# Optimization experiments

Hardware: AMD Instinct MI355X
Metric: run time of the kernel (lower is better)

Reference implementation:

```python
import jax, jax.numpy as jnp
import numpy as np

N = 100000
E = 1600000
NODE_IN = 8
EDGE_IN = 4
HID = 64
OUT = 4

# torch-initialized skip weights, in usage order (w2_1..w7_7)
SKIP_INIT = np.array([0.6, 0.4,
                      0.6, 0.4, 0.2,
                      0.6, 0.4, 0.2, 0.2,
                      0.6, 0.4, 0.2, 0.2, 0.2,
                      0.6, 0.4, 0.2, 0.2, 0.2, 0.2,
                      0.6, 0.4, 0.2, 0.2, 0.2, 0.2, 0.2], dtype=np.float32)

def _lin(key, fan_in, fan_out):
    b = 1.0 / np.sqrt(fan_in)
    k1, k2 = jax.random.split(key)
    W = jax.random.uniform(k1, (fan_in, fan_out), jnp.float32, -b, b)
    bias = jax.random.uniform(k2, (fan_out,), jnp.float32, -b, b)
    return W, bias

def setup_inputs() -> dict:
    key = jax.random.key(0)
    ks = jax.random.split(key, 20)
    x = jax.random.normal(ks[0], (N, NODE_IN), jnp.float32)
    edge_index = jax.random.randint(ks[1], (2, E), 0, N, jnp.int64)
    edge_attr = jax.random.normal(ks[2], (E, EDGE_IN), jnp.float32)
    # layer1
    Wm1, bm1 = _lin(ks[3], NODE_IN + EDGE_IN, HID)
    Wu1, bu1 = _lin(ks[4], NODE_IN + HID, HID)
    # mid layers (layers 2..6 of the torch module; layer7 is never used)
    Wm_mid, bm_mid, Wu_mid, bu_mid = [], [], [], []
    for i in range(5):
        Wm, bm = _lin(ks[5 + 2 * i], HID + EDGE_IN, HID)
        Wu, bu = _lin(ks[6 + 2 * i], HID + HID, HID)
        Wm_mid.append(Wm); bm_mid.append(bm); Wu_mid.append(Wu); bu_mid.append(bu)
    Wm_mid = jnp.stack(Wm_mid); bm_mid = jnp.stack(bm_mid)
    Wu_mid = jnp.stack(Wu_mid); bu_mid = jnp.stack(bu_mid)
    # last layer
    Wm_last, bm_last = _lin(ks[16], HID + EDGE_IN, OUT)
    Wu_last, bu_last = _lin(ks[17], HID + OUT, OUT)
    skip_weights = jnp.asarray(SKIP_INIT)
    return dict(x=x, edge_index=edge_index, edge_attr=edge_attr,
                Wm1=Wm1, bm1=bm1, Wu1=Wu1, bu1=bu1,
                Wm_mid=Wm_mid, bm_mid=bm_mid, Wu_mid=Wu_mid, bu_mid=bu_mid,
                Wm_last=Wm_last, bm_last=bm_last, Wu_last=Wu_last, bu_last=bu_last,
                skip_weights=skip_weights)

def _graph_layer(h, src, dst, edge_attr, Wm, bm, Wu, bu):
    # message: ReLU(Linear([h_src, e_attr]))  -> [E, out]
    m = jax.nn.relu(jnp.concatenate([h[src], edge_attr], axis=-1) @ Wm + bm)
    # sum-aggregate messages at destination nodes -> [N, out]
    agg = jax.ops.segment_sum(m, dst, num_segments=N)
    # node update: ReLU(Linear([h, agg]))
    return jax.nn.relu(jnp.concatenate([h, agg], axis=-1) @ Wu + bu)

def reference(x, edge_index, edge_attr,
              Wm1, bm1, Wu1, bu1,
              Wm_mid, bm_mid, Wu_mid, bu_mid,
              Wm_last, bm_last, Wu_last, bu_last,
              skip_weights):
    src, dst = edge_index[0], edge_index[1]
    sw = skip_weights
    L = lambda h, i: _graph_layer(h, src, dst, edge_attr,
                                  Wm_mid[i], bm_mid[i], Wu_mid[i], bu_mid[i])
    x1 = _graph_layer(x, src, dst, edge_attr, Wm1, bm1, Wu1, bu1)
    x2 = L(x1, 0)
    x2w = x1 * sw[0] + x2 * sw[1]
    x3 = L(x2w, 1)
    x3w = x1 * sw[2] + x2w * sw[3] + x3 * sw[4]
    x4 = L(x3w, 2)
    x4w = x1 * sw[5] + x2w * sw[6] + x3w * sw[7] + x4 * sw[8]
    x5 = L(x4w, 2)  # NOTE: source reuses layer4 here (faithful to bug)
    x5w = x1 * sw[9] + x2w * sw[10] + x3w * sw[11] + x4w * sw[12] + x5 * sw[13]
    x6 = L(x5w, 3)  # layer5
    x6w = x1 * sw[14] + x2w * sw[15] + x3w * sw[16] + x4w * sw[17] + x5w * sw[18] + x6 * sw[19]
    x7 = L(x6w, 4)  # layer6
    x7w = (x1 * sw[20] + x2w * sw[21] + x3w * sw[22] + x4w * sw[23]
           + x5w * sw[24] + x6w * sw[25] + x7 * sw[26])
    return _graph_layer(x7w, src, dst, edge_attr, Wm_last, bm_last, Wu_last, bu_last)
```

## Files before the change

### kernel.cpp

```cpp
#include <hip/hip_runtime.h>


#define WAVE 64

__global__ __launch_bounds__(256) void hist_kernel(
    const int* __restrict__ ei, int* __restrict__ cnt, int E)
{
    int t = blockIdx.x * blockDim.x + threadIdx.x;
    int nt = gridDim.x * blockDim.x;
    for (int e = t; e < E; e += nt) atomicAdd(&cnt[ei[E + e]], 1);
}

__global__ __launch_bounds__(256) void scan1_kernel(
    const int* __restrict__ cnt, int* __restrict__ out, int* __restrict__ bsum, int N)
{
    __shared__ int lds[256];
    int t = threadIdx.x;
    int base = blockIdx.x * 1024 + t * 4;
    int v0 = (base + 0 < N) ? cnt[base + 0] : 0;
    int v1 = (base + 1 < N) ? cnt[base + 1] : 0;
    int v2 = (base + 2 < N) ? cnt[base + 2] : 0;
    int v3 = (base + 3 < N) ? cnt[base + 3] : 0;
    int tsum = v0 + v1 + v2 + v3;
    lds[t] = tsum;
    __syncthreads();
    for (int off = 1; off < 256; off <<= 1) {
        int x = 0;
        if (t >= off) x = lds[t - off];
        __syncthreads();
        if (t >= off) lds[t] += x;
        __syncthreads();
    }
    int run = lds[t] - tsum;
    if (base + 0 < N) out[base + 0] = run; run += v0;
    if (base + 1 < N) out[base + 1] = run; run += v1;
    if (base + 2 < N) out[base + 2] = run; run += v2;
    if (base + 3 < N) out[base + 3] = run;
    if (t == 255) bsum[blockIdx.x] = lds[255];
}

__global__ __launch_bounds__(256) void scan2_kernel(int* __restrict__ bsum, int B)
{
    __shared__ int lds[256];
    __shared__ int carry;
    int t = threadIdx.x;
    if (t == 0) carry = 0;
    __syncthreads();
    for (int start = 0; start < B; start += 256) {
        int i = start + t;
        int v = (i < B) ? bsum[i] : 0;
        lds[t] = v;
        __syncthreads();
        for (int off = 1; off < 256; off <<= 1) {
            int x = 0;
            if (t >= off) x = lds[t - off];
            __syncthreads();
            if (t >= off) lds[t] += x;
            __syncthreads();
        }
        if (i < B) bsum[i] = carry + lds[t] - v;
        __syncthreads();
        if (t == 255) carry += lds[255];
        __syncthreads();
    }
}

__global__ __launch_bounds__(256) void scan3_kernel(
    int* __restrict__ rowptr, int* __restrict__ cursor,
    const int* __restrict__ bsum, int N, int E)
{
    int t = blockIdx.x * blockDim.x + threadIdx.x;
    int nt = gridDim.x * blockDim.x;
    for (int i = t; i < N; i += nt) {
        int v = rowptr[i] + bsum[i >> 10];
        rowptr[i] = v;
        cursor[i] = v;
    }
    if (t == 0) rowptr[N] = E;
}

__global__ __launch_bounds__(256) void scatter_kernel(
    const int* __restrict__ ei, const float* __restrict__ ea,
    int* __restrict__ cursor, int* __restrict__ srcp, float* __restrict__ eap, int E)
{
    int t = blockIdx.x * blockDim.x + threadIdx.x;
    int nt = gridDim.x * blockDim.x;
    for (int e = t; e < E; e += nt) {
        int d = ei[E + e];
        int pos = atomicAdd(&cursor[d], 1);
        srcp[pos] = ei[e];
        *reinterpret_cast<float4*>(eap + (size_t)4 * pos) =
            *reinterpret_cast<const float4*>(ea + (size_t)4 * e);
    }
}


template<int C>
__device__ __forceinline__ void stage_rows(
    const float* __restrict__ src, int rs, int base, int N, int t, float* As)
{
    constexpr int NFQ = C / 4;
    for (int idx = t; idx < 64 * NFQ; idx += 256) {
        int n = idx / NFQ, kq = idx % NFQ;
        int gn = min(base + n, N - 1);
        *reinterpret_cast<float4*>(As + n * 68 + 4 * kq) =
            *reinterpret_cast<const float4*>(src + (size_t)gn * rs + 4 * kq);
    }
}

template<int C>
__device__ __forceinline__ void stage_w(
    const float* __restrict__ Wg, int t, float* Ws)
{
    const float4* wsrc = reinterpret_cast<const float4*>(Wg);
    float4* wdst = reinterpret_cast<float4*>(Ws);
    for (int idx = t; idx < C * 16; idx += 256) wdst[idx] = wsrc[idx];
}

template<int C>
__device__ __forceinline__ void compute_rm(
    const float* As, const float* Ws, int tx, int ty, float acc[4][4])
{
#pragma unroll 2
    for (int k = 0; k < C; k += 4) {
        float4 w0 = *reinterpret_cast<const float4*>(Ws + (k + 0) * 64 + 4 * tx);
        float4 w1 = *reinterpret_cast<const float4*>(Ws + (k + 1) * 64 + 4 * tx);
        float4 w2 = *reinterpret_cast<const float4*>(Ws + (k + 2) * 64 + 4 * tx);
        float4 w3 = *reinterpret_cast<const float4*>(Ws + (k + 3) * 64 + 4 * tx);
#pragma unroll
        for (int i = 0; i < 4; ++i) {
            float4 a = *reinterpret_cast<const float4*>(As + (4 * ty + i) * 68 + k);
            acc[i][0] = fmaf(a.x, w0.x, acc[i][0]);
            acc[i][1] = fmaf(a.x, w0.y, acc[i][1]);
            acc[i][2] = fmaf(a.x, w0.z, acc[i][2]);
            acc[i][3] = fmaf(a.x, w0.w, acc[i][3]);
            acc[i][0] = fmaf(a.y, w1.x, acc[i][0]);
            acc[i][1] = fmaf(a.y, w1.y, acc[i][1]);
            acc[i][2] = fmaf(a.y, w1.z, acc[i][2]);
            acc[i][3] = fmaf(a.y, w1.w, acc[i][3]);
            acc[i][0] = fmaf(a.z, w2.x, acc[i][0]);
            acc[i][1] = fmaf(a.z, w2.y, acc[i][1]);
            acc[i][2] = fmaf(a.z, w2.z, acc[i][2]);
            acc[i][3] = fmaf(a.z, w2.w, acc[i][3]);
            acc[i][0] = fmaf(a.w, w3.x, acc[i][0]);
            acc[i][1] = fmaf(a.w, w3.y, acc[i][1]);
            acc[i][2] = fmaf(a.w, w3.z, acc[i][2]);
            acc[i][3] = fmaf(a.w, w3.w, acc[i][3]);
        }
    }
}

template<int K1, bool HASB, bool RELU, bool SKIPP, bool UPDP, bool INITP>
__global__ __launch_bounds__(256) void lin3_kernel(
    const float* __restrict__ A, const float* __restrict__ B,
    const float* __restrict__ W, const float* __restrict__ bias,
    float* __restrict__ out, float* __restrict__ P, int N,
    const float* __restrict__ sw, int csIdx, int ciIdx)
{
    __shared__ float As[64 * 68];
    __shared__ float Ws[64 * 64];
    int t = threadIdx.x;
    int tx = t & 15, ty = t >> 4;
    int base = blockIdx.x * 64;

    float acc[4][4];
    {
        float4 bv = *reinterpret_cast<const float4*>(bias + 4 * tx);
#pragma unroll
        for (int i = 0; i < 4; ++i) {
            acc[i][0] = bv.x; acc[i][1] = bv.y; acc[i][2] = bv.z; acc[i][3] = bv.w;
        }
    }

    stage_rows<K1>(A, K1, base, N, t, As);
    stage_w<K1>(W, t, Ws);
    __syncthreads();
    compute_rm<K1>(As, Ws, tx, ty, acc);

    if constexpr (HASB) {
        __syncthreads();
        stage_rows<64>(B, 64, base, N, t, As);
        stage_w<64>(W + (size_t)K1 * 64, t, Ws);
        __syncthreads();
        compute_rm<64>(As, Ws, tx, ty, acc);
    }

    float cs = 0.0f, ci = 0.0f;
    if (SKIPP) cs = sw[csIdx];
    if (UPDP || INITP) ci = sw[ciIdx];

#pragma unroll
    for (int i = 0; i < 4; ++i) {
        int gn = base + 4 * ty + i;
        if (gn >= N) continue;
        float r0 = acc[i][0], r1 = acc[i][1], r2 = acc[i][2], r3 = acc[i][3];
        if (RELU) {
            r0 = fmaxf(r0, 0.0f); r1 = fmaxf(r1, 0.0f);
            r2 = fmaxf(r2, 0.0f); r3 = fmaxf(r3, 0.0f);
        }
        size_t off = (size_t)gn * 64 + 4 * tx;
        float4 Pv;
        if (SKIPP) {
            Pv = *reinterpret_cast<const float4*>(P + off);
            r0 = fmaf(cs, r0, Pv.x);
            r1 = fmaf(cs, r1, Pv.y);
            r2 = fmaf(cs, r2, Pv.z);
            r3 = fmaf(cs, r3, Pv.w);
        }
        float4 r; r.x = r0; r.y = r1; r.z = r2; r.w = r3;
        *reinterpret_cast<float4*>(out + off) = r;
        if (UPDP) {
            float4 Pn;
            Pn.x = fmaf(ci, r0, Pv.x);
            Pn.y = fmaf(ci, r1, Pv.y);
            Pn.z = fmaf(ci, r2, Pv.z);
            Pn.w = fmaf(ci, r3, Pv.w);
            *reinterpret_cast<float4*>(P + off) = Pn;
        }
        if (INITP) {
            float4 Pn;
            Pn.x = ci * r0; Pn.y = ci * r1; Pn.z = ci * r2; Pn.w = ci * r3;
            *reinterpret_cast<float4*>(P + off) = Pn;
        }
    }
}

__global__ __launch_bounds__(256) void csr_agg_kernel(
    const int* __restrict__ rowptr, const int* __restrict__ srcp,
    const float* __restrict__ eap, const float* __restrict__ p,
    const float* __restrict__ Wme, float* __restrict__ agg, int N)
{
    int lane = threadIdx.x & 63;
    int g = lane >> 4;
    int q = lane & 15;
    int gwave = blockIdx.x * (blockDim.x >> 6) + (threadIdx.x >> 6);
    int nw = gridDim.x * (blockDim.x >> 6);
    float4 w0 = *reinterpret_cast<const float4*>(Wme + 0 * 64 + 4 * q);
    float4 w1 = *reinterpret_cast<const float4*>(Wme + 1 * 64 + 4 * q);
    float4 w2 = *reinterpret_cast<const float4*>(Wme + 2 * 64 + 4 * q);
    float4 w3 = *reinterpret_cast<const float4*>(Wme + 3 * 64 + 4 * q);

    for (int n = gwave; n < N; n += nw) {
        int beg = rowptr[n], end = rowptr[n + 1];
        int deg = end - beg;
        int nc = (deg + 3) >> 2;
        float4 acc = {0, 0, 0, 0};
        int sA = 0, sB = 0;
        float4 aA = {0, 0, 0, 0}, aB = {0, 0, 0, 0};
        bool vA = (g < deg);
        bool vB = (4 + g < deg);
        if (vA) { sA = srcp[beg + g];     aA = *reinterpret_cast<const float4*>(eap + (size_t)4 * (beg + g)); }
        if (vB) { sB = srcp[beg + 4 + g]; aB = *reinterpret_cast<const float4*>(eap + (size_t)4 * (beg + 4 + g)); }
        float4 pA = *reinterpret_cast<const float4*>(p + (size_t)sA * 64 + 4 * q);
        for (int c = 0; c < nc; ++c) {
            int sC = 0; float4 aC = {0, 0, 0, 0};
            bool vC = (4 * (c + 2) + g) < deg;
            if (vC) {
                int jc = beg + 4 * (c + 2) + g;
                sC = srcp[jc];
                aC = *reinterpret_cast<const float4*>(eap + (size_t)4 * jc);
            }
            float4 pB = *reinterpret_cast<const float4*>(p + (size_t)sB * 64 + 4 * q);
            float4 m;
            m.x = fmaf(aA.x, w0.x, fmaf(aA.y, w1.x, fmaf(aA.z, w2.x, fmaf(aA.w, w3.x, pA.x))));
            m.y = fmaf(aA.x, w0.y, fmaf(aA.y, w1.y, fmaf(aA.z, w2.y, fmaf(aA.w, w3.y, pA.y))));
            m.z = fmaf(aA.x, w0.z, fmaf(aA.y, w1.z, fmaf(aA.z, w2.z, fmaf(aA.w, w3.z, pA.z))));
            m.w = fmaf(aA.x, w0.w, fmaf(aA.y, w1.w, fmaf(aA.z, w2.w, fmaf(aA.w, w3.w, pA.w))));
            float f = vA ? 1.0f : 0.0f;
            acc.x = fmaf(f, fmaxf(m.x, 0.0f), acc.x);
            acc.y = fmaf(f, fmaxf(m.y, 0.0f), acc.y);
            acc.z = fmaf(f, fmaxf(m.z, 0.0f), acc.z);
            acc.w = fmaf(f, fmaxf(m.w, 0.0f), acc.w);
            vA = vB; aA = aB; pA = pB;
            vB = vC; aB = aC; sB = sC;
        }
        acc.x += __shfl_xor(acc.x, 16); acc.y += __shfl_xor(acc.y, 16);
        acc.z += __shfl_xor(acc.z, 16); acc.w += __shfl_xor(acc.w, 16);
        acc.x += __shfl_xor(acc.x, 32); acc.y += __shfl_xor(acc.y, 32);
        acc.z += __shfl_xor(acc.z, 32); acc.w += __shfl_xor(acc.w, 32);
        if (g == 0)
            *reinterpret_cast<float4*>(agg + (size_t)n * 64 + 4 * q) = acc;
    }
}

__global__ __launch_bounds__(256) void edge_kernel(
    const int* __restrict__ ei, const float* __restrict__ ea,
    const float* __restrict__ p, const float* __restrict__ Wme,
    float* __restrict__ agg, int E)
{
    int lane = threadIdx.x & 63;
    int gwave = blockIdx.x * (blockDim.x >> 6) + (threadIdx.x >> 6);
    int nw = gridDim.x * (blockDim.x >> 6);
    float w0 = Wme[0 * 64 + lane];
    float w1 = Wme[1 * 64 + lane];
    float w2 = Wme[2 * 64 + lane];
    float w3 = Wme[3 * 64 + lane];
    for (int e = gwave; e < E; e += nw) {
        int s = ei[e];
        int d = ei[E + e];
        float4 a = *reinterpret_cast<const float4*>(ea + (size_t)4 * e);
        float v = p[(size_t)s * 64 + lane];
        v = fmaf(a.x, w0, v);
        v = fmaf(a.y, w1, v);
        v = fmaf(a.z, w2, v);
        v = fmaf(a.w, w3, v);
        v = fmaxf(v, 0.0f);
        atomicAdd(agg + (size_t)d * 64 + lane, v);
    }
}

__global__ __launch_bounds__(256) void skipinit_kernel(
    const float* __restrict__ xin, float* __restrict__ P,
    const float* __restrict__ sw, int ciIdx, int n64)
{
    float ci = sw[ciIdx];
    int t = blockIdx.x * blockDim.x + threadIdx.x;
    int nt = gridDim.x * blockDim.x;
    for (int i = t; i < n64; i += nt) P[i] = ci * xin[i];
}

__global__ __launch_bounds__(256) void pl_kernel(
    const float* __restrict__ A, const float* __restrict__ W,
    const float* __restrict__ bias, float* __restrict__ out, int N)
{
    __shared__ float Wl[64 * 4];
    __shared__ float bl[4];
    for (int i = threadIdx.x; i < 256; i += blockDim.x) Wl[i] = W[i];
    if (threadIdx.x < 4) bl[threadIdx.x] = bias[threadIdx.x];
    __syncthreads();
    int t = blockIdx.x * blockDim.x + threadIdx.x;
    int nt = gridDim.x * blockDim.x;
    for (int idx = t; idx < N * 4; idx += nt) {
        int n = idx >> 2, f = idx & 3;
        float acc = bl[f];
        const float* ar = A + (size_t)n * 64;
#pragma unroll 4
        for (int kk = 0; kk < 16; ++kk) {
            float4 a4 = *reinterpret_cast<const float4*>(ar + 4 * kk);
            acc = fmaf(a4.x, Wl[(4 * kk + 0) * 4 + f], acc);
            acc = fmaf(a4.y, Wl[(4 * kk + 1) * 4 + f], acc);
            acc = fmaf(a4.z, Wl[(4 * kk + 2) * 4 + f], acc);
            acc = fmaf(a4.w, Wl[(4 * kk + 3) * 4 + f], acc);
        }
        out[idx] = acc;
    }
}

__global__ __launch_bounds__(256) void csr_agg4_kernel(
    const int* __restrict__ rowptr, const int* __restrict__ srcp,
    const float* __restrict__ eap, const float* __restrict__ p4,
    const float* __restrict__ Wme, float* __restrict__ agg4, int N)
{
    float w[16];
#pragma unroll
    for (int i = 0; i < 16; ++i) w[i] = Wme[i];
    int t = blockIdx.x * blockDim.x + threadIdx.x;
    int nt = gridDim.x * blockDim.x;
    for (int n = t; n < N; n += nt) {
        int beg = rowptr[n], end = rowptr[n + 1];
        float4 acc = {0, 0, 0, 0};
        for (int j = beg; j < end; ++j) {
            int s = srcp[j];
            float4 a = *reinterpret_cast<const float4*>(eap + (size_t)4 * j);
            float4 pv = *reinterpret_cast<const float4*>(p4 + (size_t)4 * s);
            float vx = pv.x + a.x * w[0] + a.y * w[4] + a.z * w[8]  + a.w * w[12];
            float vy = pv.y + a.x * w[1] + a.y * w[5] + a.z * w[9]  + a.w * w[13];
            float vz = pv.z + a.x * w[2] + a.y * w[6] + a.z * w[10] + a.w * w[14];
            float vw = pv.w + a.x * w[3] + a.y * w[7] + a.z * w[11] + a.w * w[15];
            acc.x += fmaxf(vx, 0.0f);
            acc.y += fmaxf(vy, 0.0f);
            acc.z += fmaxf(vz, 0.0f);
            acc.w += fmaxf(vw, 0.0f);
        }
        *reinterpret_cast<float4*>(agg4 + (size_t)4 * n) = acc;
    }
}

__global__ __launch_bounds__(256) void edge4_kernel(
    const int* __restrict__ ei, const float* __restrict__ ea,
    const float* __restrict__ p4, const float* __restrict__ Wme,
    float* __restrict__ agg4, int E)
{
    int lane = threadIdx.x & 63;
    int f = lane & 3;
    int gwave = blockIdx.x * (blockDim.x >> 6) + (threadIdx.x >> 6);
    int nw = gridDim.x * (blockDim.x >> 6);
    float w0 = Wme[0 * 4 + f];
    float w1 = Wme[1 * 4 + f];
    float w2 = Wme[2 * 4 + f];
    float w3 = Wme[3 * 4 + f];
    for (int e0 = gwave * 16; e0 < E; e0 += nw * 16) {
        int e = e0 + (lane >> 2);
        if (e < E) {
            int s = ei[e];
            int d = ei[E + e];
            float4 a = *reinterpret_cast<const float4*>(ea + (size_t)4 * e);
            float v = p4[(size_t)s * 4 + f];
            v = fmaf(a.x, w0, v);
            v = fmaf(a.y, w1, v);
            v = fmaf(a.z, w2, v);
            v = fmaf(a.w, w3, v);
            v = fmaxf(v, 0.0f);
            atomicAdd(agg4 + (size_t)d * 4 + f, v);
        }
    }
}

__global__ __launch_bounds__(256) void ul_kernel(
    const float* __restrict__ A, const float* __restrict__ agg4,
    const float* __restrict__ W , const float* __restrict__ bias,
    float* __restrict__ out, int N)
{
    __shared__ float Wl[68 * 4];
    __shared__ float bl[4];
    for (int i = threadIdx.x; i < 68 * 4; i += blockDim.x) Wl[i] = W[i];
    if (threadIdx.x < 4) bl[threadIdx.x] = bias[threadIdx.x];
    __syncthreads();
    int t = blockIdx.x * blockDim.x + threadIdx.x;
    int nt = gridDim.x * blockDim.x;
    for (int idx = t; idx < N * 4; idx += nt) {
        int n = idx >> 2, f = idx & 3;
        float acc = bl[f];
        const float* ar = A + (size_t)n * 64;
#pragma unroll 4
        for (int kk = 0; kk < 16; ++kk) {
            float4 a4 = *reinterpret_cast<const float4*>(ar + 4 * kk);
            acc = fmaf(a4.x, Wl[(4 * kk + 0) * 4 + f], acc);
            acc = fmaf(a4.y, Wl[(4 * kk + 1) * 4 + f], acc);
            acc = fmaf(a4.z, Wl[(4 * kk + 2) * 4 + f], acc);
            acc = fmaf(a4.w, Wl[(4 * kk + 3) * 4 + f], acc);
        }
        float4 g = *reinterpret_cast<const float4*>(agg4 + (size_t)n * 4);
        acc = fmaf(g.x, Wl[(64 + 0) * 4 + f], acc);
        acc = fmaf(g.y, Wl[(64 + 1) * 4 + f], acc);
        acc = fmaf(g.z, Wl[(64 + 2) * 4 + f], acc);
        acc = fmaf(g.w, Wl[(64 + 3) * 4 + f], acc);
        out[idx] = fmaxf(acc, 0.0f);
    }
}

extern "C" void kernel_launch(void* const* d_in, const int* in_sizes, int n_in,
                              void* d_out, int out_size, void* d_ws, size_t ws_size,
                              hipStream_t stream)
{
    const float* x      = (const float*)d_in[0];
    const int*   ei     = (const int*)d_in[1];
    const float* ea     = (const float*)d_in[2];
    const float* Wm1    = (const float*)d_in[3];
    const float* bm1    = (const float*)d_in[4];
    const float* Wu1    = (const float*)d_in[5];
    const float* bu1    = (const float*)d_in[6];
    const float* Wm_mid = (const float*)d_in[7];
    const float* bm_mid = (const float*)d_in[8];
    const float* Wu_mid = (const float*)d_in[9];
    const float* bu_mid = (const float*)d_in[10];
    const float* WmL    = (const float*)d_in[11];
    const float* bmL    = (const float*)d_in[12];
    const float* WuL    = (const float*)d_in[13];
    const float* buL    = (const float*)d_in[14];
    const float* sw     = (const float*)d_in[15];

    const int N = in_sizes[0] / 8;
    const int E = in_sizes[2] / 4;

    float* ws = (float*)d_ws;
    size_t nh = (size_t)N * 64;
    float* p    = ws;
    float* agg  = ws + nh;
    float* xwA  = ws + 2 * nh;
    float* xwB  = ws + 3 * nh;
    float* P    = ws + 4 * nh;
    float* p4   = agg;
    float* agg4 = agg + (size_t)N * 4;

    float* eap   = ws + 5 * nh;
    int*   srcp  = (int*)(eap + (size_t)E * 4);
    int*   rowptr= srcp + E;
    int*   cursor= rowptr + N + 1;
    int*   bsum  = cursor + N;
    size_t need_bytes = (5 * nh + (size_t)E * 4) * 4 + ((size_t)E + 2 * N + 1 + 1024) * 4;
    bool use_csr = ws_size >= need_bytes;

    dim3 blk(256);
    dim3 gEdge(2048), g4(1024);
    dim3 gLin((N + 63) / 64);
    const float* nul = nullptr;

    if (use_csr) {
        int B = (N + 1023) / 1024;
        hipMemsetAsync(cursor, 0, (size_t)N * 4, stream);
        hist_kernel<<<gEdge, blk, 0, stream>>>(ei, cursor, E);
        scan1_kernel<<<dim3(B), blk, 0, stream>>>(cursor, rowptr, bsum, N);
        scan2_kernel<<<dim3(1), blk, 0, stream>>>(bsum, B);
        scan3_kernel<<<dim3(256), blk, 0, stream>>>(rowptr, cursor, bsum, N, E);
        scatter_kernel<<<gEdge, blk, 0, stream>>>(ei, ea, cursor, srcp, eap, E);
    }

    auto edge_pass = [&](const float* pp, const float* Wme, float* aggout) {
        if (use_csr) {
            csr_agg_kernel<<<gEdge, blk, 0, stream>>>(rowptr, srcp, eap, pp, Wme, aggout, N);
        } else {
            hipMemsetAsync(aggout, 0, nh * sizeof(float), stream);
            edge_kernel<<<gEdge, blk, 0, stream>>>(ei, ea, pp, Wme, aggout, E);
        }
    };

    struct MidStep { int mi; const float* in; float* out; int cs; int ci; };
    MidStep steps[6] = {
        {0, xwA, xwB, 1,  3},
        {1, xwB, xwA, 4,  7},
        {2, xwA, xwB, 8,  12},
        {2, xwB, xwA, 13, 18},
        {3, xwA, xwB, 19, 25},
        {4, xwB, xwA, 26, 0},
    };

    lin3_kernel<8, false, false, false, false, false><<<gLin, blk, 0, stream>>>(
        x, nul, Wm1, bm1, p, nullptr, N, sw, 0, 0);
    edge_pass(p, Wm1 + 8 * 64, agg);
    lin3_kernel<8, true, true, false, false, true><<<gLin, blk, 0, stream>>>(
        x, agg, Wu1, bu1, xwA, P, N, sw, 0, 0);

    for (int li = 0; li < 6; ++li) {
        const MidStep& st = steps[li];
        const float* Wm = Wm_mid + (size_t)st.mi * 68 * 64;
        const float* bm = bm_mid + (size_t)st.mi * 64;
        const float* Wu = Wu_mid + (size_t)st.mi * 128 * 64;
        const float* bu = bu_mid + (size_t)st.mi * 64;
        lin3_kernel<64, false, false, false, false, false><<<gLin, blk, 0, stream>>>(
            st.in, nul, Wm, bm, p, nullptr, N, sw, 0, 0);
        edge_pass(p, Wm + 64 * 64, agg);
        if (li < 5) {
            lin3_kernel<64, true, true, true, true, false><<<gLin, blk, 0, stream>>>(
                st.in, agg, Wu, bu, st.out, P, N, sw, st.cs, st.ci);
        } else {
            lin3_kernel<64, true, true, true, false, false><<<gLin, blk, 0, stream>>>(
                st.in, agg, Wu, bu, st.out, P, N, sw, st.cs, 0);
        }
    }
    float* x7w = steps[5].out;

    pl_kernel<<<g4, blk, 0, stream>>>(x7w, WmL, bmL, p4, N);
    if (use_csr) {
        csr_agg4_kernel<<<g4, blk, 0, stream>>>(rowptr, srcp, eap, p4, WmL + 64 * 4, agg4, N);
    } else {
        hipMemsetAsync(agg4, 0, (size_t)N * 4 * sizeof(float), stream);
        edge4_kernel<<<gEdge, blk, 0, stream>>>(ei, ea, p4, WmL + 64 * 4, agg4, E);
    }
    ul_kernel<<<g4, blk, 0, stream>>>(x7w, agg4, WuL, buL, (float*)d_out, N);
}
```

Baseline: 1.014 ms.

## Fuse next layer's message projection into the update linear kernel epilogue

The update linear kernel now keeps its output tile in shared memory and immediately multiplies it by the next layer's message weight matrix, writing the projected features p. This removes the separate message-projection launch per mid layer and the re-read of the freshly written node features from global memory. In exchange it adds a third weight stage and a second GEMM per block, plus extra register and LDS pressure. The unused skipinit kernel is also deleted.

```diff
diff --git a/kernel.cpp b/kernel.cpp
--- a/kernel.cpp
+++ b/kernel.cpp
@@ -150,11 +150,13 @@
     }
 }
 
-template<int K1, bool HASB, bool RELU, bool SKIPP, bool UPDP, bool INITP>
-__global__ __launch_bounds__(256) void lin3_kernel(
+template<int K1, bool HASB, bool RELU, bool SKIPP, bool UPDP, bool INITP, bool HASP>
+__global__ __launch_bounds__(256) void lin4_kernel(
     const float* __restrict__ A, const float* __restrict__ B,
     const float* __restrict__ W, const float* __restrict__ bias,
-    float* __restrict__ out, float* __restrict__ P, int N,
+    float* __restrict__ out, float* __restrict__ P,
+    const float* __restrict__ Wnext, const float* __restrict__ bnext,
+    float* __restrict__ pout, int N,
     const float* __restrict__ sw, int csIdx, int ciIdx)
 {
     __shared__ float As[64 * 68];
@@ -189,38 +191,67 @@
     if (SKIPP) cs = sw[csIdx];
     if (UPDP || INITP) ci = sw[ciIdx];
 
+    if constexpr (HASP) __syncthreads();
+
 #pragma unroll
     for (int i = 0; i < 4; ++i) {
         int gn = base + 4 * ty + i;
-        if (gn >= N) continue;
         float r0 = acc[i][0], r1 = acc[i][1], r2 = acc[i][2], r3 = acc[i][3];
         if (RELU) {
             r0 = fmaxf(r0, 0.0f); r1 = fmaxf(r1, 0.0f);
             r2 = fmaxf(r2, 0.0f); r3 = fmaxf(r3, 0.0f);
         }
         size_t off = (size_t)gn * 64 + 4 * tx;
-        float4 Pv;
-        if (SKIPP) {
+        float4 Pv = {0, 0, 0, 0};
+        if (SKIPP && gn < N) {
             Pv = *reinterpret_cast<const float4*>(P + off);
             r0 = fmaf(cs, r0, Pv.x);
             r1 = fmaf(cs, r1, Pv.y);
             r2 = fmaf(cs, r2, Pv.z);
             r3 = fmaf(cs, r3, Pv.w);
         }
-        float4 r; r.x = r0; r.y = r1; r.z = r2; r.w = r3;
-        *reinterpret_cast<float4*>(out + off) = r;
-        if (UPDP) {
-            float4 Pn;
-            Pn.x = fmaf(ci, r0, Pv.x);
-            Pn.y = fmaf(ci, r1, Pv.y);
-            Pn.z = fmaf(ci, r2, Pv.z);
-            Pn.w = fmaf(ci, r3, Pv.w);
-            *reinterpret_cast<float4*>(P + off) = Pn;
-        }
-        if (INITP) {
-            float4 Pn;
-            Pn.x = ci * r0; Pn.y = ci * r1; Pn.z = ci * r2; Pn.w = ci * r3;
-            *reinterpret_cast<float4*>(P + off) = Pn;
+        if (gn < N) {
+            float4 r; r.x = r0; r.y = r1; r.z = r2; r.w = r3;
+            *reinterpret_cast<float4*>(out + off) = r;
+            if (UPDP) {
+                float4 Pn;
+                Pn.x = fmaf(ci, r0, Pv.x);
+                Pn.y = fmaf(ci, r1, Pv.y);
+                Pn.z = fmaf(ci, r2, Pv.z);
+                Pn.w = fmaf(ci, r3, Pv.w);
+                *reinterpret_cast<float4*>(P + off) = Pn;
+            }
+            if (INITP) {
+                float4 Pn;
+                Pn.x = ci * r0; Pn.y = ci * r1; Pn.z = ci * r2; Pn.w = ci * r3;
+                *reinterpret_cast<float4*>(P + off) = Pn;
+            }
+        }
+        if (HASP) {
+            float* as = As + (4 * ty + i) * 68 + 4 * tx;
+            as[0] = r0; as[1] = r1; as[2] = r2; as[3] = r3;
+        }
+    }
+
+    if constexpr (HASP) {
+        stage_w<64>(Wnext, t, Ws);
+        __syncthreads();
+        float acc2[4][4];
+        {
+            float4 bv = *reinterpret_cast<const float4*>(bnext + 4 * tx);
+#pragma unroll
+            for (int i = 0; i < 4; ++i) {
+                acc2[i][0] = bv.x; acc2[i][1] = bv.y; acc2[i][2] = bv.z; acc2[i][3] = bv.w;
+            }
+        }
+        compute_rm<64>(As, Ws, tx, ty, acc2);
+#pragma unroll
+        for (int i = 0; i < 4; ++i) {
+            int gn = base + 4 * ty + i;
+            if (gn < N) {
+                float4 r; r.x = acc2[i][0]; r.y = acc2[i][1]; r.z = acc2[i][2]; r.w = acc2[i][3];
+                *reinterpret_cast<float4*>(pout + (size_t)gn * 64 + 4 * tx) = r;
+            }
         }
     }
 }
@@ -309,16 +340,6 @@
     }
 }
 
-__global__ __launch_bounds__(256) void skipinit_kernel(
-    const float* __restrict__ xin, float* __restrict__ P,
-    const float* __restrict__ sw, int ciIdx, int n64)
-{
-    float ci = sw[ciIdx];
-    int t = blockIdx.x * blockDim.x + threadIdx.x;
-    int nt = gridDim.x * blockDim.x;
-    for (int i = t; i < n64; i += nt) P[i] = ci * xin[i];
-}
-
 __global__ __launch_bounds__(256) void pl_kernel(
     const float* __restrict__ A, const float* __restrict__ W,
     const float* __restrict__ bias, float* __restrict__ out, int N)
@@ -515,27 +536,29 @@
         {4, xwB, xwA, 26, 0},
     };
 
-    lin3_kernel<8, false, false, false, false, false><<<gLin, blk, 0, stream>>>(
-        x, nul, Wm1, bm1, p, nullptr, N, sw, 0, 0);
+    lin4_kernel<8, false, false, false, false, false, false><<<gLin, blk, 0, stream>>>(
+        x, nul, Wm1, bm1, p, nullptr, nul, nul, nullptr, N, sw, 0, 0);
     edge_pass(p, Wm1 + 8 * 64, agg);
-    lin3_kernel<8, true, true, false, false, true><<<gLin, blk, 0, stream>>>(
-        x, agg, Wu1, bu1, xwA, P, N, sw, 0, 0);
+    lin4_kernel<8, true, true, false, false, true, true><<<gLin, blk, 0, stream>>>(
+        x, agg, Wu1, bu1, xwA, P,
+        Wm_mid + (size_t)0 * 68 * 64, bm_mid + (size_t)0 * 64, p, N, sw, 0, 0);
 
     for (int li = 0; li < 6; ++li) {
         const MidStep& st = steps[li];
         const float* Wm = Wm_mid + (size_t)st.mi * 68 * 64;
-        const float* bm = bm_mid + (size_t)st.mi * 64;
         const float* Wu = Wu_mid + (size_t)st.mi * 128 * 64;
         const float* bu = bu_mid + (size_t)st.mi * 64;
-        lin3_kernel<64, false, false, false, false, false><<<gLin, blk, 0, stream>>>(
-            st.in, nul, Wm, bm, p, nullptr, N, sw, 0, 0);
         edge_pass(p, Wm + 64 * 64, agg);
         if (li < 5) {
-            lin3_kernel<64, true, true, true, true, false><<<gLin, blk, 0, stream>>>(
-                st.in, agg, Wu, bu, st.out, P, N, sw, st.cs, st.ci);
+            int nmi = steps[li + 1].mi;
+            lin4_kernel<64, true, true, true, true, false, true><<<gLin, blk, 0, stream>>>(
+                st.in, agg, Wu, bu, st.out, P,
+                Wm_mid + (size_t)nmi * 68 * 64, bm_mid + (size_t)nmi * 64, p, N,
+                sw, st.cs, st.ci);
         } else {
-            lin3_kernel<64, true, true, true, false, false><<<gLin, blk, 0, stream>>>(
-                st.in, agg, Wu, bu, st.out, P, N, sw, st.cs, 0);
+            lin4_kernel<64, true, true, true, false, false, false><<<gLin, blk, 0, stream>>>(
+                st.in, agg, Wu, bu, st.out, P,
+                nul, nul, nullptr, N, sw, st.cs, 0);
         }
     }
     float* x7w = steps[5].out;
```

Measured after the change: 969.6 us. -4.3%, faster.
